# Performance work log

Measured on AMD Instinct MI355X. Metric: run time of the kernel, lower is better.

Reference implementation:

```python
import jax, jax.numpy as jnp
import numpy as np

N = 1024
E = 16384
F_IN = 128
H = 64
ALPHA = 0.7


def _gcn(x, src, dst, W, b):
    # PyG GCNConv: add self-loops, symmetric deg^{-1/2} normalization, aggregate at dst.
    loop = jnp.arange(N)
    s = jnp.concatenate([src, loop])
    d = jnp.concatenate([dst, loop])
    deg = jax.ops.segment_sum(jnp.ones_like(s, jnp.float32), d, num_segments=N)
    dinv = jnp.where(deg > 0, jax.lax.rsqrt(deg), 0.0)
    norm = dinv[s] * dinv[d]  # [E+N]
    h = x @ W  # [N,H]
    out = jax.ops.segment_sum(norm[:, None] * h[s], d, num_segments=N)
    return out + b


def _gat(x, src, dst, ew, W, a_src, a_dst, w_edge, a_edge, b):
    # PyG GATConv (heads=1) with scalar edge_attr via lin_edge(edge_dim=1).
    h = x @ W  # [N,H]
    al_s = h @ a_src  # [N]
    al_d = h @ a_dst  # [N]
    loop = jnp.arange(N)
    s = jnp.concatenate([src, loop])
    d = jnp.concatenate([dst, loop])
    ew_l = jnp.concatenate([ew, jnp.full((N,), jnp.mean(ew))])  # fill_value='mean' for self-loops
    c = jnp.dot(w_edge, a_edge)  # scalar: (lin_edge(ew) * att_edge).sum() = ew * c
    e = jax.nn.leaky_relu(al_s[s] + al_d[d] + ew_l * c, 0.2)  # [E+N]
    # segment softmax over destination nodes (every node has a self-loop -> no empty segments)
    emax = jax.ops.segment_max(e, d, num_segments=N)
    ex = jnp.exp(e - emax[d])
    denom = jax.ops.segment_sum(ex, d, num_segments=N)
    alpha = ex / denom[d]
    out = jax.ops.segment_sum(alpha[:, None] * h[s], d, num_segments=N)
    return out + b


def setup_inputs() -> dict:
    key = jax.random.key(0)
    ks = jax.random.split(key, 24)
    g = lambda k, shape, fan: jax.random.normal(k, shape, jnp.float32) / np.sqrt(fan)
    inp = {
        "x": jax.random.normal(ks[0], (N, F_IN), jnp.float32),
        "edge_index_above": jax.random.randint(ks[1], (2, E), 0, N),
        "edge_index_distance": jax.random.randint(ks[2], (2, E), 0, N),
        "edge_weights_distance": jax.random.uniform(ks[3], (E,), jnp.float32),
        # GCNConv1 / GATConv1 (in 128 -> 64)
        "W_gcn1": g(ks[4], (F_IN, H), F_IN), "b_gcn1": jnp.zeros((H,), jnp.float32),
        "W_gat1": g(ks[5], (F_IN, H), F_IN), "att_src1": g(ks[6], (H,), H),
        "att_dst1": g(ks[7], (H,), H), "w_edge1": g(ks[8], (H,), 1),
        "att_edge1": g(ks[9], (H,), H), "b_gat1": jnp.zeros((H,), jnp.float32),
        # GCNConv2 / GATConv2 (64 -> 64)
        "W_gcn2": g(ks[10], (H, H), H), "b_gcn2": jnp.zeros((H,), jnp.float32),
        "W_gat2": g(ks[11], (H, H), H), "att_src2": g(ks[12], (H,), H),
        "att_dst2": g(ks[13], (H,), H), "w_edge2": g(ks[14], (H,), 1),
        "att_edge2": g(ks[15], (H,), H), "b_gat2": jnp.zeros((H,), jnp.float32),
        # GCNConv3 (64 -> 64)
        "W_gcn3": g(ks[16], (H, H), H), "b_gcn3": jnp.zeros((H,), jnp.float32),
        # predictor MLP: Linear(128,64) -> ReLU -> Linear(64,1) -> Sigmoid
        "Wp1": g(ks[17], (2 * H, H), 2 * H), "bp1": jnp.zeros((H,), jnp.float32),
        "Wp2": g(ks[18], (H, 1), H), "bp2": jnp.zeros((1,), jnp.float32),
    }
    return inp


def reference(x, edge_index_above, edge_index_distance, edge_weights_distance,
              W_gcn1, b_gcn1, W_gat1, att_src1, att_dst1, w_edge1, att_edge1, b_gat1,
              W_gcn2, b_gcn2, W_gat2, att_src2, att_dst2, w_edge2, att_edge2, b_gat2,
              W_gcn3, b_gcn3, Wp1, bp1, Wp2, bp2):
    sa, da = edge_index_above[0], edge_index_above[1]
    sd, dd = edge_index_distance[0], edge_index_distance[1]
    ew = edge_weights_distance

    xa1 = jax.nn.relu(_gcn(x, sa, da, W_gcn1, b_gcn1))
    xd1 = jax.nn.relu(_gat(x, sd, dd, ew, W_gat1, att_src1, att_dst1, w_edge1, att_edge1, b_gat1))
    xa2 = jax.nn.relu(_gcn(xa1, sa, da, W_gcn2, b_gcn2))
    xd2 = jax.nn.relu(_gat(xd1, sd, dd, ew, W_gat2, att_src2, att_dst2, w_edge2, att_edge2, b_gat2))
    xc = ALPHA * xa2 + (1.0 - ALPHA) * xd2
    h = jax.nn.relu(_gcn(xc, sa, da, W_gcn3, b_gcn3))  # [N,H]

    # All-pairs predictor, fused: concat([h_i, h_j]) @ Wp1 = h_i @ Wp1[:H] + h_j @ Wp1[H:]
    h1 = h @ Wp1[:H]  # [N,H] contribution of start node
    h2 = h @ Wp1[H:]  # [N,H] contribution of end node
    pre = jax.nn.relu(h1[:, None, :] + h2[None, :, :] + bp1)  # [N,N,H]
    logits = jnp.einsum('ijh,h->ij', pre, Wp2[:, 0]) + bp2[0]  # [N,N]
    return jax.nn.sigmoid(logits).reshape(-1)  # [N*N], row-major = cartesian_prod order
```

## Files before the change

### kernel.cpp

```cpp
#include <hip/hip_runtime.h>

constexpr int NV  = 1024;
constexpr int EV  = 16384;
constexpr int FIN = 128;
constexpr int HD  = 64;
constexpr int CAP = 64;

__device__ __forceinline__ float relu_(float v){ return fmaxf(v, 0.f); }

__device__ __forceinline__ float wsum64(float v){
    for (int off = 32; off; off >>= 1) v += __shfl_xor(v, off, 64);
    return v;
}

struct KArgs {
    const float* x;
    const int *sa, *da, *sd, *dd;
    const float* ew;
    const float *Wg1, *bg1;
    const float *Wt1, *as1, *ad1, *we1, *ae1, *bt1;
    const float *Wg2, *bg2;
    const float *Wt2, *as2, *ad2, *we2, *ae2, *bt2;
    const float *Wg3, *bg3;
    const float *Wp1, *bp1, *Wp2, *bp2;
    int *cnt_a, *cnt_d;
    float* scal;
    float *al_s1, *al_d1, *al_s2, *al_d2;
    int *ell_a, *ell_d;
    float* ellw_d;
    float *hg1, *hga1, *hg2, *hga2, *hg3, *h1, *h2;
    float* out;
};

__device__ __forceinline__ float gcn_row_w(const KArgs& A, const float* __restrict__ h,
                                           const float* __restrict__ bias, int d, int k)
{
    int deg = min(A.cnt_a[d], CAP);
    int   s_l = A.ell_a[d*CAP + k];
    s_l = (k < deg) ? s_l : 0;
    float c_l = (k < deg) ? rsqrtf((float)A.cnt_a[s_l] + 1.f) : 0.f;
    float dv  = rsqrtf((float)deg + 1.f);
    float a0 = dv * h[d*HD + k], a1 = 0.f, a2 = 0.f, a3 = 0.f;
    int degR = (deg + 3) & ~3;
    for (int p = 0; p < degR; p += 4) {
        int   s0 = __shfl(s_l, p,   64), s1 = __shfl(s_l, p+1, 64),
              s2 = __shfl(s_l, p+2, 64), s3 = __shfl(s_l, p+3, 64);
        float c0 = __shfl(c_l, p,   64), c1 = __shfl(c_l, p+1, 64),
              c2 = __shfl(c_l, p+2, 64), c3 = __shfl(c_l, p+3, 64);
        a0 = fmaf(c0, h[s0*HD + k], a0);
        a1 = fmaf(c1, h[s1*HD + k], a1);
        a2 = fmaf(c2, h[s2*HD + k], a2);
        a3 = fmaf(c3, h[s3*HD + k], a3);
    }
    return relu_(fmaf(dv, (a0+a1) + (a2+a3), bias[k]));
}

__device__ __forceinline__ float gat_row_w(const KArgs& A, const float* __restrict__ h,
                                           const float* __restrict__ bias,
                                           const float* __restrict__ al_s,
                                           const float* __restrict__ al_d,
                                           float c, float ewm, int d, int k)
{
    int deg = min(A.cnt_d[d], CAP);
    float aD = al_d[d];
    int   s_l = A.ell_d[d*CAP + k];
    float w_l = A.ellw_d[d*CAP + k];
    s_l = (k < deg) ? s_l : 0;
    float e_l = al_s[s_l] + aD + w_l*c;
    e_l = (e_l > 0.f) ? e_l : 0.2f*e_l;
    float x_l = (k < deg) ? expf(e_l) : 0.f;
    float es  = al_s[d] + aD + ewm*c;
    es = expf((es > 0.f) ? es : 0.2f*es);
    float den = es + wsum64(x_l);
    float n0 = es * h[d*HD + k], n1 = 0.f, n2 = 0.f, n3 = 0.f;
    int degR = (deg + 3) & ~3;
    for (int p = 0; p < degR; p += 4) {
        int   s0 = __shfl(s_l, p,   64), s1 = __shfl(s_l, p+1, 64),
              s2 = __shfl(s_l, p+2, 64), s3 = __shfl(s_l, p+3, 64);
        float x0 = __shfl(x_l, p,   64), x1 = __shfl(x_l, p+1, 64),
              x2 = __shfl(x_l, p+2, 64), x3 = __shfl(x_l, p+3, 64);
        n0 = fmaf(x0, h[s0*HD + k], n0);
        n1 = fmaf(x1, h[s1*HD + k], n1);
        n2 = fmaf(x2, h[s2*HD + k], n2);
        n3 = fmaf(x3, h[s3*HD + k], n3);
    }
    return relu_(((n0+n1) + (n2+n3))/den + bias[k]);
}

__device__ __forceinline__ float mm_row_lds(const float4* __restrict__ rowF4,
                                            const float* __restrict__ Wf, int j)
{
    float acc = 0.f;
    #pragma unroll
    for (int k4 = 0; k4 < 16; k4++) {
        float4 r = rowF4[k4];
        acc = fmaf(r.x, Wf[(4*k4+0)*64 + j], acc);
        acc = fmaf(r.y, Wf[(4*k4+1)*64 + j], acc);
        acc = fmaf(r.z, Wf[(4*k4+2)*64 + j], acc);
        acc = fmaf(r.w, Wf[(4*k4+3)*64 + j], acc);
    }
    return acc;
}

__global__ __launch_bounds__(256) void k1(KArgs A)
{
    __shared__ __align__(16) float4 Ws[FIN*16];
    const int b = blockIdx.x, tid = threadIdx.x;
    if (b < 512) {
        bool gcn = (b < 256);
        const float4* Wsrc = (const float4*)(gcn ? A.Wg1 : A.Wt1);
        for (int r = tid; r < FIN*16; r += 256) Ws[r] = Wsrc[r];
        __syncthreads();
        int t = (gcn ? b : b-256)*256 + tid, i = t >> 6, j = t & 63;
        const float4* xr = (const float4*)(A.x + i*FIN);
        const float*  Wf = (const float*)Ws;
        float acc = 0.f;
        #pragma unroll
        for (int k4 = 0; k4 < FIN/4; k4++) {
            float4 xv = xr[k4];
            acc = fmaf(xv.x, Wf[(4*k4+0)*64 + j], acc);
            acc = fmaf(xv.y, Wf[(4*k4+1)*64 + j], acc);
            acc = fmaf(xv.z, Wf[(4*k4+2)*64 + j], acc);
            acc = fmaf(xv.w, Wf[(4*k4+3)*64 + j], acc);
        }
        if (gcn) {
            A.hg1[t] = acc;
        } else {
            A.hga1[t] = acc;
            float ps = acc * A.as1[j];
            float pd = acc * A.ad1[j];
            for (int off = 32; off; off >>= 1) {
                ps += __shfl_down(ps, off, 64);
                pd += __shfl_down(pd, off, 64);
            }
            if (j == 0) { A.al_s1[i] = ps; A.al_d1[i] = pd; }
        }
    } else if (b < 576) {
        int e = (b-512)*256 + tid;
        int dA = A.da[e], dD = A.dd[e];
        int pa = atomicAdd(&A.cnt_a[dA], 1);
        if (pa < CAP) A.ell_a[dA*CAP + pa] = A.sa[e];
        float w = A.ew[e];
        int pd = atomicAdd(&A.cnt_d[dD], 1);
        if (pd < CAP) { A.ell_d[dD*CAP + pd] = A.sd[e]; A.ellw_d[dD*CAP + pd] = w; }
        for (int off = 32; off; off >>= 1) w += __shfl_down(w, off, 64);
        if ((tid & 63) == 0) atomicAdd(&A.scal[3], w);
    } else {
        if (tid < 64) {
            float p1 = A.we1[tid]*A.ae1[tid];
            float p2 = A.we2[tid]*A.ae2[tid];
            for (int off = 32; off; off >>= 1) {
                p1 += __shfl_down(p1, off, 64);
                p2 += __shfl_down(p2, off, 64);
            }
            if (tid == 0) { A.scal[1] = p1; A.scal[2] = p2; }
        }
    }
}

__global__ __launch_bounds__(256) void k2(KArgs A)
{
    __shared__ __align__(16) float4 Ws[HD*16];
    __shared__ float rowb[4*64];
    const int b = blockIdx.x, tid = threadIdx.x;
    const float4* Wsrc = (const float4*)((b < 256) ? A.Wg2 : A.Wt2);
    for (int r = tid; r < HD*16; r += 256) Ws[r] = Wsrc[r];
    __syncthreads();
    int w = tid >> 6, k = tid & 63;
    const float* Wf = (const float*)Ws;
    if (b < 256) {
        int d = b*4 + w;
        rowb[w*64 + k] = gcn_row_w(A, A.hg1, A.bg1, d, k);
        A.hg2[d*HD + k] = mm_row_lds((const float4*)(rowb + w*64), Wf, k);
    } else {
        int i = (b-256)*4 + w;
        float c = A.scal[1], ewm = A.scal[3] * (1.f/EV);
        rowb[w*64 + k] = gat_row_w(A, A.hga1, A.bt1, A.al_s1, A.al_d1,
                                   c, ewm, i, k);
        float acc = mm_row_lds((const float4*)(rowb + w*64), Wf, k);
        A.hga2[i*HD + k] = acc;
        float ps = acc * A.as2[k];
        float pd = acc * A.ad2[k];
        for (int off = 32; off; off >>= 1) {
            ps += __shfl_down(ps, off, 64);
            pd += __shfl_down(pd, off, 64);
        }
        if (k == 0) { A.al_s2[i] = ps; A.al_d2[i] = pd; }
    }
}

__global__ __launch_bounds__(256) void k3(KArgs A)
{
    __shared__ __align__(16) float4 Ws[HD*16];
    __shared__ float rows[4*64];
    const int b = blockIdx.x, tid = threadIdx.x;
    for (int r = tid; r < HD*16; r += 256) Ws[r] = ((const float4*)A.Wg3)[r];
    int w = tid >> 6, k = tid & 63;
    int node = b*2 + (w >> 1);
    float v;
    if ((w & 1) == 0) {
        v = 0.7f * gcn_row_w(A, A.hg2, A.bg2, node, k);
    } else {
        float c = A.scal[2], ewm = A.scal[3] * (1.f/EV);
        v = 0.3f * gat_row_w(A, A.hga2, A.bt2, A.al_s2, A.al_d2,
                             c, ewm, node, k);
    }
    rows[w*64 + k] = v;
    __syncthreads();
    if ((w & 1) == 0) {
        const float* Wf = (const float*)Ws;
        const float4* r0 = (const float4*)(rows + w*64);
        const float4* r1 = (const float4*)(rows + (w+1)*64);
        float acc = 0.f;
        #pragma unroll
        for (int k4 = 0; k4 < 16; k4++) {
            float4 ra = r0[k4], rb = r1[k4];
            acc = fmaf(ra.x+rb.x, Wf[(4*k4+0)*64 + k], acc);
            acc = fmaf(ra.y+rb.y, Wf[(4*k4+1)*64 + k], acc);
            acc = fmaf(ra.z+rb.z, Wf[(4*k4+2)*64 + k], acc);
            acc = fmaf(ra.w+rb.w, Wf[(4*k4+3)*64 + k], acc);
        }
        A.hg3[node*HD + k] = acc;
    }
}

__global__ __launch_bounds__(256) void k4(KArgs A)
{
    __shared__ __align__(16) float4 Wp[FIN*16];
    __shared__ float rowb[4*64];
    const int b = blockIdx.x, tid = threadIdx.x;
    for (int r = tid; r < FIN*16; r += 256) Wp[r] = ((const float4*)A.Wp1)[r];
    __syncthreads();
    int w = tid >> 6, k = tid & 63;
    int d = b*4 + w;
    rowb[w*64 + k] = gcn_row_w(A, A.hg3, A.bg3, d, k);
    const float*  Wf = (const float*)Wp;
    const float4* rF = (const float4*)(rowb + w*64);
    float a1 = 0.f, a2 = 0.f;
    #pragma unroll
    for (int k4i = 0; k4i < 16; k4i++) {
        float4 r = rF[k4i];
        a1 = fmaf(r.x, Wf[(4*k4i+0)*64 + k], a1);
        a2 = fmaf(r.x, Wf[(64+4*k4i+0)*64 + k], a2);
        a1 = fmaf(r.y, Wf[(4*k4i+1)*64 + k], a1);
        a2 = fmaf(r.y, Wf[(64+4*k4i+1)*64 + k], a2);
        a1 = fmaf(r.z, Wf[(4*k4i+2)*64 + k], a1);
        a2 = fmaf(r.z, Wf[(64+4*k4i+2)*64 + k], a2);
        a1 = fmaf(r.w, Wf[(4*k4i+3)*64 + k], a1);
        a2 = fmaf(r.w, Wf[(64+4*k4i+3)*64 + k], a2);
    }
    A.h1[d*HD + k] = a1 + A.bp1[k];
    A.h2[d*HD + k] = a2;
}

__global__ __launch_bounds__(256) void k5(KArgs A)
{
    __shared__ float4 s1[32*17], s2[32*17], w2s[16];
    const int tid = threadIdx.x;
    int by = blockIdx.x >> 5, bx = blockIdx.x & 31;
    int i0 = by*32, j0 = bx*32;
    for (int r = tid; r < 512; r += 256) {
        int row = r >> 4, c = r & 15;
        s1[row*17 + c] = ((const float4*)A.h1)[(i0+row)*16 + c];
        s2[row*17 + c] = ((const float4*)A.h2)[(j0+row)*16 + c];
    }
    if (tid < 16) w2s[tid] = ((const float4*)A.Wp2)[tid];
    __syncthreads();
    int ty = tid >> 4, tx = tid & 15;
    float a00=0.f, a01=0.f, a10=0.f, a11=0.f;
    #pragma unroll
    for (int k4 = 0; k4 < 16; k4++) {
        float4 va0 = s1[ty*17 + k4],      va1 = s1[(ty+16)*17 + k4];
        float4 vb0 = s2[tx*17 + k4],      vb1 = s2[(tx+16)*17 + k4];
        float4 wv  = w2s[k4];
#define STEP(c) \
        a00 = fmaf(fmaxf(va0.c+vb0.c, 0.f), wv.c, a00); \
        a01 = fmaf(fmaxf(va0.c+vb1.c, 0.f), wv.c, a01); \
        a10 = fmaf(fmaxf(va1.c+vb0.c, 0.f), wv.c, a10); \
        a11 = fmaf(fmaxf(va1.c+vb1.c, 0.f), wv.c, a11);
        STEP(x) STEP(y) STEP(z) STEP(w)
#undef STEP
    }
    float bb = A.bp2[0];
    int i = i0 + ty, jj = j0 + tx;
    A.out[i*NV + jj]            = 1.f/(1.f + expf(-(a00+bb)));
    A.out[i*NV + jj + 16]       = 1.f/(1.f + expf(-(a01+bb)));
    A.out[(i+16)*NV + jj]       = 1.f/(1.f + expf(-(a10+bb)));
    A.out[(i+16)*NV + jj + 16]  = 1.f/(1.f + expf(-(a11+bb)));
}

extern "C" void kernel_launch(void* const* d_in, const int* in_sizes, int n_in,
                              void* d_out, int out_size, void* d_ws, size_t ws_size,
                              hipStream_t stream)
{
    KArgs A;
    A.x   = (const float*)d_in[0];
    const int* ei_a = (const int*)d_in[1];
    const int* ei_d = (const int*)d_in[2];
    A.ew  = (const float*)d_in[3];
    A.Wg1 = (const float*)d_in[4];  A.bg1 = (const float*)d_in[5];
    A.Wt1 = (const float*)d_in[6];  A.as1 = (const float*)d_in[7];
    A.ad1 = (const float*)d_in[8];  A.we1 = (const float*)d_in[9];
    A.ae1 = (const float*)d_in[10]; A.bt1 = (const float*)d_in[11];
    A.Wg2 = (const float*)d_in[12]; A.bg2 = (const float*)d_in[13];
    A.Wt2 = (const float*)d_in[14]; A.as2 = (const float*)d_in[15];
    A.ad2 = (const float*)d_in[16]; A.we2 = (const float*)d_in[17];
    A.ae2 = (const float*)d_in[18]; A.bt2 = (const float*)d_in[19];
    A.Wg3 = (const float*)d_in[20]; A.bg3 = (const float*)d_in[21];
    A.Wp1 = (const float*)d_in[22]; A.bp1 = (const float*)d_in[23];
    A.Wp2 = (const float*)d_in[24]; A.bp2 = (const float*)d_in[25];
    A.sa = ei_a;      A.da = ei_a + EV;
    A.sd = ei_d;      A.dd = ei_d + EV;
    A.out = (float*)d_out;

    float* W = (float*)d_ws;
    A.cnt_a  = (int*)(W + 0);
    A.cnt_d  = (int*)(W + 1024);
    A.scal   = W + 2048;
    A.al_s1  = W + 2064;
    A.al_d1  = W + 3088;
    A.al_s2  = W + 4112;
    A.al_d2  = W + 5136;
    A.ell_a  = (int*)(W + 6160);
    A.ell_d  = (int*)(W + 71696);
    A.ellw_d = W + 137232;
    A.hg1    = W + 202768;
    A.hga1   = W + 268304;
    A.hg2    = W + 333840;
    A.hga2   = W + 399376;
    A.hg3    = W + 464912;
    A.h1     = W + 530448;
    A.h2     = W + 595984;

    hipMemsetAsync(d_ws, 0, 2064*sizeof(float), stream);

    k1<<<577,  256, 0, stream>>>(A);
    k2<<<512,  256, 0, stream>>>(A);
    k3<<<512,  256, 0, stream>>>(A);
    k4<<<256,  256, 0, stream>>>(A);
    k5<<<1024, 256, 0, stream>>>(A);
}
```

Measured before the change: 144.9 us.

## Fuse five stage kernels into one persistent kernel with software grid barriers

Replaces the five separate launches with a single 1024-block kernel that runs every stage and separates them with a hierarchical atomic grid barrier (32 sub-counters feeding one global counter). The aim is to remove the launch gaps and tail drain between the small dependent stages. In exchange, all 1024 blocks must be co-resident (launch bounds of 4 blocks per CU with about 33 KB of LDS each), and some stages leave most blocks idle at the barriers. The barrier also has a spin-count timeout, which could silently break ordering if residency is not met.

```diff
diff --git a/kernel.cpp b/kernel.cpp
--- a/kernel.cpp
+++ b/kernel.cpp
@@ -5,6 +5,7 @@
 constexpr int FIN = 128;
 constexpr int HD  = 64;
 constexpr int CAP = 64;
+constexpr int GRID = 1024;
 
 __device__ __forceinline__ float relu_(float v){ return fmaxf(v, 0.f); }
 
@@ -25,12 +26,32 @@
     const float *Wp1, *bp1, *Wp2, *bp2;
     int *cnt_a, *cnt_d;
     float* scal;
+    int*   bar;
     float *al_s1, *al_d1, *al_s2, *al_d2;
     int *ell_a, *ell_d;
     float* ellw_d;
     float *hg1, *hga1, *hg2, *hga2, *hg3, *h1, *h2;
     float* out;
 };
+
+__device__ __forceinline__ void gridbar(int* __restrict__ bar, int phase)
+{
+    __syncthreads();
+    if (threadIdx.x == 0) {
+        __threadfence();
+        const int tgt = 32 * phase;
+        if (atomicAdd(&bar[(blockIdx.x & 31) << 4], 1) == tgt - 1)
+            atomicAdd(&bar[512], 1);
+        int spins = 0;
+        while (__hip_atomic_load(&bar[512], __ATOMIC_RELAXED,
+                                 __HIP_MEMORY_SCOPE_AGENT) < tgt) {
+            __builtin_amdgcn_s_sleep(16);
+            if (++spins > (1 << 17)) break;
+        }
+        __threadfence();
+    }
+    __syncthreads();
+}
 
 __device__ __forceinline__ float gcn_row_w(const KArgs& A, const float* __restrict__ h,
                                            const float* __restrict__ bias, int d, int k)
@@ -102,26 +123,31 @@
     return acc;
 }
 
-__global__ __launch_bounds__(256) void k1(KArgs A)
-{
-    __shared__ __align__(16) float4 Ws[FIN*16];
+__global__ __launch_bounds__(256, 4) void fused(KArgs A)
+{
+    __shared__ __align__(16) unsigned char smem[33792];
+    float4*      WsF4 = (float4*)smem;
+    const float* Wsf  = (const float*)smem;
+    float*       rowb = (float*)(smem + 32768);
+
     const int b = blockIdx.x, tid = threadIdx.x;
+    const int w = tid >> 6, k = tid & 63;
+
     if (b < 512) {
         bool gcn = (b < 256);
         const float4* Wsrc = (const float4*)(gcn ? A.Wg1 : A.Wt1);
-        for (int r = tid; r < FIN*16; r += 256) Ws[r] = Wsrc[r];
+        for (int r = tid; r < FIN*16; r += 256) WsF4[r] = Wsrc[r];
         __syncthreads();
         int t = (gcn ? b : b-256)*256 + tid, i = t >> 6, j = t & 63;
         const float4* xr = (const float4*)(A.x + i*FIN);
-        const float*  Wf = (const float*)Ws;
         float acc = 0.f;
         #pragma unroll
         for (int k4 = 0; k4 < FIN/4; k4++) {
             float4 xv = xr[k4];
-            acc = fmaf(xv.x, Wf[(4*k4+0)*64 + j], acc);
-            acc = fmaf(xv.y, Wf[(4*k4+1)*64 + j], acc);
-            acc = fmaf(xv.z, Wf[(4*k4+2)*64 + j], acc);
-            acc = fmaf(xv.w, Wf[(4*k4+3)*64 + j], acc);
+            acc = fmaf(xv.x, Wsf[(4*k4+0)*64 + j], acc);
+            acc = fmaf(xv.y, Wsf[(4*k4+1)*64 + j], acc);
+            acc = fmaf(xv.z, Wsf[(4*k4+2)*64 + j], acc);
+            acc = fmaf(xv.w, Wsf[(4*k4+3)*64 + j], acc);
         }
         if (gcn) {
             A.hg1[t] = acc;
@@ -140,12 +166,12 @@
         int dA = A.da[e], dD = A.dd[e];
         int pa = atomicAdd(&A.cnt_a[dA], 1);
         if (pa < CAP) A.ell_a[dA*CAP + pa] = A.sa[e];
-        float w = A.ew[e];
+        float wv = A.ew[e];
         int pd = atomicAdd(&A.cnt_d[dD], 1);
-        if (pd < CAP) { A.ell_d[dD*CAP + pd] = A.sd[e]; A.ellw_d[dD*CAP + pd] = w; }
-        for (int off = 32; off; off >>= 1) w += __shfl_down(w, off, 64);
-        if ((tid & 63) == 0) atomicAdd(&A.scal[3], w);
-    } else {
+        if (pd < CAP) { A.ell_d[dD*CAP + pd] = A.sd[e]; A.ellw_d[dD*CAP + pd] = wv; }
+        for (int off = 32; off; off >>= 1) wv += __shfl_down(wv, off, 64);
+        if ((tid & 63) == 0) atomicAdd(&A.scal[3], wv);
+    } else if (b == 576) {
         if (tid < 64) {
             float p1 = A.we1[tid]*A.ae1[tid];
             float p2 = A.we2[tid]*A.ae2[tid];
@@ -156,137 +182,122 @@
             if (tid == 0) { A.scal[1] = p1; A.scal[2] = p2; }
         }
     }
-}
-
-__global__ __launch_bounds__(256) void k2(KArgs A)
-{
-    __shared__ __align__(16) float4 Ws[HD*16];
-    __shared__ float rowb[4*64];
-    const int b = blockIdx.x, tid = threadIdx.x;
-    const float4* Wsrc = (const float4*)((b < 256) ? A.Wg2 : A.Wt2);
-    for (int r = tid; r < HD*16; r += 256) Ws[r] = Wsrc[r];
-    __syncthreads();
-    int w = tid >> 6, k = tid & 63;
-    const float* Wf = (const float*)Ws;
+    gridbar(A.bar, 1);
+
+    if (b < 512) {
+        const float4* Wsrc = (const float4*)((b < 256) ? A.Wg2 : A.Wt2);
+        for (int r = tid; r < HD*16; r += 256) WsF4[r] = Wsrc[r];
+        __syncthreads();
+        if (b < 256) {
+            int d = b*4 + w;
+            rowb[w*64 + k] = gcn_row_w(A, A.hg1, A.bg1, d, k);
+            A.hg2[d*HD + k] = mm_row_lds((const float4*)(rowb + w*64), Wsf, k);
+        } else {
+            int i = (b-256)*4 + w;
+            float c = A.scal[1], ewm = A.scal[3] * (1.f/EV);
+            rowb[w*64 + k] = gat_row_w(A, A.hga1, A.bt1, A.al_s1, A.al_d1,
+                                       c, ewm, i, k);
+            float acc = mm_row_lds((const float4*)(rowb + w*64), Wsf, k);
+            A.hga2[i*HD + k] = acc;
+            float ps = acc * A.as2[k];
+            float pd = acc * A.ad2[k];
+            for (int off = 32; off; off >>= 1) {
+                ps += __shfl_down(ps, off, 64);
+                pd += __shfl_down(pd, off, 64);
+            }
+            if (k == 0) { A.al_s2[i] = ps; A.al_d2[i] = pd; }
+        }
+    }
+    gridbar(A.bar, 2);
+
+    if (b < 512) {
+        for (int r = tid; r < HD*16; r += 256) WsF4[r] = ((const float4*)A.Wg3)[r];
+        int node = b*2 + (w >> 1);
+        float v;
+        if ((w & 1) == 0) {
+            v = 0.7f * gcn_row_w(A, A.hg2, A.bg2, node, k);
+        } else {
+            float c = A.scal[2], ewm = A.scal[3] * (1.f/EV);
+            v = 0.3f * gat_row_w(A, A.hga2, A.bt2, A.al_s2, A.al_d2,
+                                 c, ewm, node, k);
+        }
+        rowb[w*64 + k] = v;
+        __syncthreads();
+        if ((w & 1) == 0) {
+            const float4* r0 = (const float4*)(rowb + w*64);
+            const float4* r1 = (const float4*)(rowb + (w+1)*64);
+            float acc = 0.f;
+            #pragma unroll
+            for (int k4 = 0; k4 < 16; k4++) {
+                float4 ra = r0[k4], rb = r1[k4];
+                acc = fmaf(ra.x+rb.x, Wsf[(4*k4+0)*64 + k], acc);
+                acc = fmaf(ra.y+rb.y, Wsf[(4*k4+1)*64 + k], acc);
+                acc = fmaf(ra.z+rb.z, Wsf[(4*k4+2)*64 + k], acc);
+                acc = fmaf(ra.w+rb.w, Wsf[(4*k4+3)*64 + k], acc);
+            }
+            A.hg3[node*HD + k] = acc;
+        }
+    }
+    gridbar(A.bar, 3);
+
     if (b < 256) {
+        for (int r = tid; r < FIN*16; r += 256) WsF4[r] = ((const float4*)A.Wp1)[r];
+        __syncthreads();
         int d = b*4 + w;
-        rowb[w*64 + k] = gcn_row_w(A, A.hg1, A.bg1, d, k);
-        A.hg2[d*HD + k] = mm_row_lds((const float4*)(rowb + w*64), Wf, k);
-    } else {
-        int i = (b-256)*4 + w;
-        float c = A.scal[1], ewm = A.scal[3] * (1.f/EV);
-        rowb[w*64 + k] = gat_row_w(A, A.hga1, A.bt1, A.al_s1, A.al_d1,
-                                   c, ewm, i, k);
-        float acc = mm_row_lds((const float4*)(rowb + w*64), Wf, k);
-        A.hga2[i*HD + k] = acc;
-        float ps = acc * A.as2[k];
-        float pd = acc * A.ad2[k];
-        for (int off = 32; off; off >>= 1) {
-            ps += __shfl_down(ps, off, 64);
-            pd += __shfl_down(pd, off, 64);
-        }
-        if (k == 0) { A.al_s2[i] = ps; A.al_d2[i] = pd; }
-    }
-}
-
-__global__ __launch_bounds__(256) void k3(KArgs A)
-{
-    __shared__ __align__(16) float4 Ws[HD*16];
-    __shared__ float rows[4*64];
-    const int b = blockIdx.x, tid = threadIdx.x;
-    for (int r = tid; r < HD*16; r += 256) Ws[r] = ((const float4*)A.Wg3)[r];
-    int w = tid >> 6, k = tid & 63;
-    int node = b*2 + (w >> 1);
-    float v;
-    if ((w & 1) == 0) {
-        v = 0.7f * gcn_row_w(A, A.hg2, A.bg2, node, k);
-    } else {
-        float c = A.scal[2], ewm = A.scal[3] * (1.f/EV);
-        v = 0.3f * gat_row_w(A, A.hga2, A.bt2, A.al_s2, A.al_d2,
-                             c, ewm, node, k);
-    }
-    rows[w*64 + k] = v;
-    __syncthreads();
-    if ((w & 1) == 0) {
-        const float* Wf = (const float*)Ws;
-        const float4* r0 = (const float4*)(rows + w*64);
-        const float4* r1 = (const float4*)(rows + (w+1)*64);
-        float acc = 0.f;
+        rowb[w*64 + k] = gcn_row_w(A, A.hg3, A.bg3, d, k);
+        const float4* rF = (const float4*)(rowb + w*64);
+        float a1 = 0.f, a2 = 0.f;
+        #pragma unroll
+        for (int k4i = 0; k4i < 16; k4i++) {
+            float4 r = rF[k4i];
+            a1 = fmaf(r.x, Wsf[(4*k4i+0)*64 + k], a1);
+            a2 = fmaf(r.x, Wsf[(64+4*k4i+0)*64 + k], a2);
+            a1 = fmaf(r.y, Wsf[(4*k4i+1)*64 + k], a1);
+            a2 = fmaf(r.y, Wsf[(64+4*k4i+1)*64 + k], a2);
+            a1 = fmaf(r.z, Wsf[(4*k4i+2)*64 + k], a1);
+            a2 = fmaf(r.z, Wsf[(64+4*k4i+2)*64 + k], a2);
+            a1 = fmaf(r.w, Wsf[(4*k4i+3)*64 + k], a1);
+            a2 = fmaf(r.w, Wsf[(64+4*k4i+3)*64 + k], a2);
+        }
+        A.h1[d*HD + k] = a1 + A.bp1[k];
+        A.h2[d*HD + k] = a2;
+    }
+    gridbar(A.bar, 4);
+
+    {
+        float4* s1  = (float4*)smem;
+        float4* s2  = (float4*)(smem + 8704);
+        float4* w2s = (float4*)(smem + 17408);
+        int i0 = (b >> 5) * 32, j0 = (b & 31) * 32;
+        for (int r = tid; r < 512; r += 256) {
+            int row = r >> 4, c = r & 15;
+            s1[row*17 + c] = ((const float4*)A.h1)[(i0+row)*16 + c];
+            s2[row*17 + c] = ((const float4*)A.h2)[(j0+row)*16 + c];
+        }
+        if (tid < 16) w2s[tid] = ((const float4*)A.Wp2)[tid];
+        __syncthreads();
+        int ty = tid >> 4, tx = tid & 15;
+        float a00=0.f, a01=0.f, a10=0.f, a11=0.f;
         #pragma unroll
         for (int k4 = 0; k4 < 16; k4++) {
-            float4 ra = r0[k4], rb = r1[k4];
-            acc = fmaf(ra.x+rb.x, Wf[(4*k4+0)*64 + k], acc);
-            acc = fmaf(ra.y+rb.y, Wf[(4*k4+1)*64 + k], acc);
-            acc = fmaf(ra.z+rb.z, Wf[(4*k4+2)*64 + k], acc);
-            acc = fmaf(ra.w+rb.w, Wf[(4*k4+3)*64 + k], acc);
-        }
-        A.hg3[node*HD + k] = acc;
-    }
-}
-
-__global__ __launch_bounds__(256) void k4(KArgs A)
-{
-    __shared__ __align__(16) float4 Wp[FIN*16];
-    __shared__ float rowb[4*64];
-    const int b = blockIdx.x, tid = threadIdx.x;
-    for (int r = tid; r < FIN*16; r += 256) Wp[r] = ((const float4*)A.Wp1)[r];
-    __syncthreads();
-    int w = tid >> 6, k = tid & 63;
-    int d = b*4 + w;
-    rowb[w*64 + k] = gcn_row_w(A, A.hg3, A.bg3, d, k);
-    const float*  Wf = (const float*)Wp;
-    const float4* rF = (const float4*)(rowb + w*64);
-    float a1 = 0.f, a2 = 0.f;
-    #pragma unroll
-    for (int k4i = 0; k4i < 16; k4i++) {
-        float4 r = rF[k4i];
-        a1 = fmaf(r.x, Wf[(4*k4i+0)*64 + k], a1);
-        a2 = fmaf(r.x, Wf[(64+4*k4i+0)*64 + k], a2);
-        a1 = fmaf(r.y, Wf[(4*k4i+1)*64 + k], a1);
-        a2 = fmaf(r.y, Wf[(64+4*k4i+1)*64 + k], a2);
-        a1 = fmaf(r.z, Wf[(4*k4i+2)*64 + k], a1);
-        a2 = fmaf(r.z, Wf[(64+4*k4i+2)*64 + k], a2);
-        a1 = fmaf(r.w, Wf[(4*k4i+3)*64 + k], a1);
-        a2 = fmaf(r.w, Wf[(64+4*k4i+3)*64 + k], a2);
-    }
-    A.h1[d*HD + k] = a1 + A.bp1[k];
-    A.h2[d*HD + k] = a2;
-}
-
-__global__ __launch_bounds__(256) void k5(KArgs A)
-{
-    __shared__ float4 s1[32*17], s2[32*17], w2s[16];
-    const int tid = threadIdx.x;
-    int by = blockIdx.x >> 5, bx = blockIdx.x & 31;
-    int i0 = by*32, j0 = bx*32;
-    for (int r = tid; r < 512; r += 256) {
-        int row = r >> 4, c = r & 15;
-        s1[row*17 + c] = ((const float4*)A.h1)[(i0+row)*16 + c];
-        s2[row*17 + c] = ((const float4*)A.h2)[(j0+row)*16 + c];
-    }
-    if (tid < 16) w2s[tid] = ((const float4*)A.Wp2)[tid];
-    __syncthreads();
-    int ty = tid >> 4, tx = tid & 15;
-    float a00=0.f, a01=0.f, a10=0.f, a11=0.f;
-    #pragma unroll
-    for (int k4 = 0; k4 < 16; k4++) {
-        float4 va0 = s1[ty*17 + k4],      va1 = s1[(ty+16)*17 + k4];
-        float4 vb0 = s2[tx*17 + k4],      vb1 = s2[(tx+16)*17 + k4];
-        float4 wv  = w2s[k4];
+            float4 va0 = s1[ty*17 + k4],      va1 = s1[(ty+16)*17 + k4];
+            float4 vb0 = s2[tx*17 + k4],      vb1 = s2[(tx+16)*17 + k4];
+            float4 wv  = w2s[k4];
 #define STEP(c) \
-        a00 = fmaf(fmaxf(va0.c+vb0.c, 0.f), wv.c, a00); \
-        a01 = fmaf(fmaxf(va0.c+vb1.c, 0.f), wv.c, a01); \
-        a10 = fmaf(fmaxf(va1.c+vb0.c, 0.f), wv.c, a10); \
-        a11 = fmaf(fmaxf(va1.c+vb1.c, 0.f), wv.c, a11);
-        STEP(x) STEP(y) STEP(z) STEP(w)
+            a00 = fmaf(fmaxf(va0.c+vb0.c, 0.f), wv.c, a00); \
+            a01 = fmaf(fmaxf(va0.c+vb1.c, 0.f), wv.c, a01); \
+            a10 = fmaf(fmaxf(va1.c+vb0.c, 0.f), wv.c, a10); \
+            a11 = fmaf(fmaxf(va1.c+vb1.c, 0.f), wv.c, a11);
+            STEP(x) STEP(y) STEP(z) STEP(w)
 #undef STEP
-    }
-    float bb = A.bp2[0];
-    int i = i0 + ty, jj = j0 + tx;
-    A.out[i*NV + jj]            = 1.f/(1.f + expf(-(a00+bb)));
-    A.out[i*NV + jj + 16]       = 1.f/(1.f + expf(-(a01+bb)));
-    A.out[(i+16)*NV + jj]       = 1.f/(1.f + expf(-(a10+bb)));
-    A.out[(i+16)*NV + jj + 16]  = 1.f/(1.f + expf(-(a11+bb)));
+        }
+        float bb = A.bp2[0];
+        int i = i0 + ty, jj = j0 + tx;
+        A.out[i*NV + jj]            = 1.f/(1.f + expf(-(a00+bb)));
+        A.out[i*NV + jj + 16]       = 1.f/(1.f + expf(-(a01+bb)));
+        A.out[(i+16)*NV + jj]       = 1.f/(1.f + expf(-(a10+bb)));
+        A.out[(i+16)*NV + jj + 16]  = 1.f/(1.f + expf(-(a11+bb)));
+    }
 }
 
 extern "C" void kernel_launch(void* const* d_in, const int* in_sizes, int n_in,
@@ -317,26 +328,23 @@
     A.cnt_a  = (int*)(W + 0);
     A.cnt_d  = (int*)(W + 1024);
     A.scal   = W + 2048;
-    A.al_s1  = W + 2064;
-    A.al_d1  = W + 3088;
-    A.al_s2  = W + 4112;
-    A.al_d2  = W + 5136;
-    A.ell_a  = (int*)(W + 6160);
-    A.ell_d  = (int*)(W + 71696);
-    A.ellw_d = W + 137232;
-    A.hg1    = W + 202768;
-    A.hga1   = W + 268304;
-    A.hg2    = W + 333840;
-    A.hga2   = W + 399376;
-    A.hg3    = W + 464912;
-    A.h1     = W + 530448;
-    A.h2     = W + 595984;
-
-    hipMemsetAsync(d_ws, 0, 2064*sizeof(float), stream);
-
-    k1<<<577,  256, 0, stream>>>(A);
-    k2<<<512,  256, 0, stream>>>(A);
-    k3<<<512,  256, 0, stream>>>(A);
-    k4<<<256,  256, 0, stream>>>(A);
-    k5<<<1024, 256, 0, stream>>>(A);
-}
+    A.bar    = (int*)(W + 2064);
+    A.al_s1  = W + 2592;
+    A.al_d1  = W + 3616;
+    A.al_s2  = W + 4640;
+    A.al_d2  = W + 5664;
+    A.ell_a  = (int*)(W + 6688);
+    A.ell_d  = (int*)(W + 72224);
+    A.ellw_d = W + 137760;
+    A.hg1    = W + 203296;
+    A.hga1   = W + 268832;
+    A.hg2    = W + 334368;
+    A.hga2   = W + 399904;
+    A.hg3    = W + 465440;
+    A.h1     = W + 530976;
+    A.h2     = W + 596512;
+
+    hipMemsetAsync(d_ws, 0, 2592*sizeof(float), stream);
+
+    fused<<<GRID, 256, 0, stream>>>(A);
+}
```

New measurement: 296.2 us. 2.04x slower.
